# Kernel tuning notes

Measured on AMD Instinct MI355X. Metric: run time of the kernel, lower is better.

The kernel has to match this reference:

```python
import jax, jax.numpy as jnp
import numpy as np

ALPHA = 0.2  # leaky relu negative slope (LinearNet default)


def _init_linear(key, fan_in, fan_out):
    kw, kb = jax.random.split(key)
    lim = 1.0 / np.sqrt(fan_in)
    W = jax.random.uniform(kw, (fan_in, fan_out), jnp.float32, -lim, lim)
    b = jax.random.uniform(kb, (fan_out,), jnp.float32, -lim, lim)
    return W, b


def setup_inputs() -> dict:
    key = jax.random.key(0)
    keys = jax.random.split(key, 8)
    B, N, F = 8, 512, 32
    x = jax.random.normal(keys[0], (B, N, F), jnp.float32)
    # fe: [2F=64 -> 64 -> 64 -> 64], all layers leaky-relu (final_linear=False)
    fe_W0, fe_b0 = _init_linear(keys[1], 2 * F, 64)
    fe_W1, fe_b1 = _init_linear(keys[2], 64, 64)
    fe_W2, fe_b2 = _init_linear(keys[3], 64, 64)
    # fn: [64 + F = 96 -> 128 -> 128 -> 32], last layer linear (final_linear=True)
    fn_W0, fn_b0 = _init_linear(keys[4], 64 + F, 128)
    fn_W1, fn_b1 = _init_linear(keys[5], 128, 128)
    fn_W2, fn_b2 = _init_linear(keys[6], 128, 32)
    return {
        "x": x,
        "fe_W0": fe_W0, "fe_b0": fe_b0,
        "fe_W1": fe_W1, "fe_b1": fe_b1,
        "fe_W2": fe_W2, "fe_b2": fe_b2,
        "fn_W0": fn_W0, "fn_b0": fn_b0,
        "fn_W1": fn_W1, "fn_b1": fn_b1,
        "fn_W2": fn_W2, "fn_b2": fn_b2,
    }


def reference(x, fe_W0, fe_b0, fe_W1, fe_b1, fe_W2, fe_b2,
              fn_W0, fn_b0, fn_W1, fn_b1, fn_W2, fn_b2):
    B, N, F = x.shape
    # all-pairs edge inputs: A[b,i,j] = concat(x[b,i], x[b,j])  (x1=repeat rows, x2=tile)
    xi = jnp.broadcast_to(x[:, :, None, :], (B, N, N, F))
    xj = jnp.broadcast_to(x[:, None, :, :], (B, N, N, F))
    A = jnp.concatenate([xi, xj], axis=-1)  # [B, N, N, 2F]
    # edge MLP fe: leaky relu after every layer (final_linear=False)
    for W, b in ((fe_W0, fe_b0), (fe_W1, fe_b1), (fe_W2, fe_b2)):
        A = jax.nn.leaky_relu(A @ W + b, negative_slope=ALPHA)
    # sum aggregation over the sender axis j
    agg = jnp.sum(A, axis=2)  # [B, N, K]
    h = jnp.concatenate([agg, x], axis=-1)  # [B, N, K + F]
    # node MLP fn: leaky relu on hidden layers, final layer linear
    h = jax.nn.leaky_relu(h @ fn_W0 + fn_b0, negative_slope=ALPHA)
    h = jax.nn.leaky_relu(h @ fn_W1 + fn_b1, negative_slope=ALPHA)
    out = h @ fn_W2 + fn_b2  # [B, N, output_node_size]
    return out
```

## Files before the change

### kernel.cpp

```cpp
#include <hip/hip_runtime.h>
#include <hip/hip_bf16.h>

#define ALPHA 0.2f
static __device__ __forceinline__ float lrel(float x) { return fmaxf(x, ALPHA * x); }

typedef __attribute__((ext_vector_type(8))) short bf16x8;
typedef __attribute__((ext_vector_type(4))) float f32x4;

union FragU { bf16x8 v; unsigned int u[4]; uint4 q; };

static __device__ __forceinline__ unsigned int pk2(float a, float b) {
    unsigned int r;
    asm("v_cvt_pk_bf16_f32 %0, %1, %2" : "=v"(r) : "v"(a), "v"(b));
    return r;
}

__global__ __launch_bounds__(256) void k_uv(
    const float* __restrict__ x, const float* __restrict__ W0, const float* __restrict__ b0,
    const float* __restrict__ W1, const float* __restrict__ W2,
    float* __restrict__ U, float* __restrict__ V, unsigned int* __restrict__ WF)
{
    if (blockIdx.x == 1024) {
        const int t = threadIdx.x;
        const int l = t & 63, part = t >> 6;
        const int lo = l & 15, g = l >> 4;
#pragma unroll
        for (int q = 0; q < 2; ++q) {
            const int ff = part * 2 + q;
            const int s = ff >> 2, nf = ff & 3;
            const int pc = 32 * (nf >> 1) + 8 * (lo >> 2) + 4 * (nf & 1) + (lo & 3);
            const int c2 = 16 * nf + lo;
            unsigned int o1[4], o2[4];
#pragma unroll
            for (int uq = 0; uq < 4; ++uq) {
                const int k0 = 32 * s + 8 * g + 2 * uq;
                o1[uq] = pk2(W1[k0 * 64 + pc], W1[(k0 + 1) * 64 + pc]);
                o2[uq] = pk2(W2[k0 * 64 + c2], W2[(k0 + 1) * 64 + c2]);
            }
            *(uint4*)(WF + (ff * 64 + l) * 4)       = make_uint4(o1[0], o1[1], o1[2], o1[3]);
            *(uint4*)(WF + ((8 + ff) * 64 + l) * 4) = make_uint4(o2[0], o2[1], o2[2], o2[3]);
        }
        return;
    }
    int idx = blockIdx.x * 256 + threadIdx.x;
    int n = idx >> 6;
    int k = idx & 63;
    const float* xr = x + n * 32;
    float u = b0[k], v = 0.f;
#pragma unroll
    for (int f = 0; f < 32; ++f) {
        float xv = xr[f];
        u += xv * W0[f * 64 + k];
        v += xv * W0[(32 + f) * 64 + k];
    }
    U[idx] = u;
    V[idx] = v;
}

__global__ __launch_bounds__(256, 2) void k_edge(
    const float* __restrict__ U, const float* __restrict__ V,
    const unsigned int* __restrict__ WF,
    const float* __restrict__ b1, const float* __restrict__ b2,
    float* __restrict__ AGG)
{
    const int tid = threadIdx.x;
    const int w = tid >> 6, l = tid & 63;
    const int lo = l & 15, g = l >> 4;
    const int bid = blockIdx.x;
    const int b = bid >> 7, ig = bid & 127;
    const int i = ig * 4 + w;
    const int node = b * 512 + i;

    FragU w1f[2][4], w2f[2][4];
    const uint4* wp = (const uint4*)WF;
#pragma unroll
    for (int s = 0; s < 2; ++s)
#pragma unroll
        for (int nf = 0; nf < 4; ++nf) {
            w1f[s][nf].q = wp[(s * 4 + nf) * 64 + l];
            w2f[s][nf].q = wp[(8 + s * 4 + nf) * 64 + l];
        }

    f32x4 b1f[4], b2f[4];
#pragma unroll
    for (int nf = 0; nf < 4; ++nf) {
        const float4 t1 = *(const float4*)(b1 + 32 * (nf >> 1) + 8 * g + 4 * (nf & 1));
        const float4 t2 = *(const float4*)(b2 + 16 * nf + 4 * g);
        b1f[nf] = (f32x4){t1.x, t1.y, t1.z, t1.w};
        b2f[nf] = (f32x4){t2.x, t2.y, t2.z, t2.w};
    }

    const float* up = U + node * 64 + 8 * g;
    const float4 ua = *(const float4*)(up);
    const float4 ub = *(const float4*)(up + 4);
    const float4 uc = *(const float4*)(up + 32);
    const float4 ud = *(const float4*)(up + 36);

    const float* Vb = V + b * 512 * 64;
    float4 vaA, vbA, vcA, vdA, vaB, vbB, vcB, vdB;
    {
        const float* pA = Vb + lo * 64 + 8 * g;
        vaA = *(const float4*)(pA);      vbA = *(const float4*)(pA + 4);
        vcA = *(const float4*)(pA + 32); vdA = *(const float4*)(pA + 36);
        const float* pB = Vb + (16 + lo) * 64 + 8 * g;
        vaB = *(const float4*)(pB);      vbB = *(const float4*)(pB + 4);
        vcB = *(const float4*)(pB + 32); vdB = *(const float4*)(pB + 36);
    }

    f32x4 agg[4];
#pragma unroll
    for (int nf = 0; nf < 4; ++nf) { f32x4 z = {0.f, 0.f, 0.f, 0.f}; agg[nf] = z; }

#pragma unroll 1
    for (int jc = 0; jc < 512; jc += 32) {
        const int jn = (jc + 32 < 512) ? jc + 32 : 0;
        const float* pA = Vb + (jn + lo) * 64 + 8 * g;
        const float4 nvaA = *(const float4*)(pA);      const float4 nvbA = *(const float4*)(pA + 4);
        const float4 nvcA = *(const float4*)(pA + 32); const float4 nvdA = *(const float4*)(pA + 36);
        const float* pB = Vb + (jn + 16 + lo) * 64 + 8 * g;
        const float4 nvaB = *(const float4*)(pB);      const float4 nvbB = *(const float4*)(pB + 4);
        const float4 nvcB = *(const float4*)(pB + 32); const float4 nvdB = *(const float4*)(pB + 36);

        FragU h0aA, h0bA, h0aB, h0bB;
        h0aA.u[0] = pk2(lrel(ua.x + vaA.x), lrel(ua.y + vaA.y));
        h0aA.u[1] = pk2(lrel(ua.z + vaA.z), lrel(ua.w + vaA.w));
        h0aA.u[2] = pk2(lrel(ub.x + vbA.x), lrel(ub.y + vbA.y));
        h0aA.u[3] = pk2(lrel(ub.z + vbA.z), lrel(ub.w + vbA.w));
        h0bA.u[0] = pk2(lrel(uc.x + vcA.x), lrel(uc.y + vcA.y));
        h0bA.u[1] = pk2(lrel(uc.z + vcA.z), lrel(uc.w + vcA.w));
        h0bA.u[2] = pk2(lrel(ud.x + vdA.x), lrel(ud.y + vdA.y));
        h0bA.u[3] = pk2(lrel(ud.z + vdA.z), lrel(ud.w + vdA.w));
        h0aB.u[0] = pk2(lrel(ua.x + vaB.x), lrel(ua.y + vaB.y));
        h0aB.u[1] = pk2(lrel(ua.z + vaB.z), lrel(ua.w + vaB.w));
        h0aB.u[2] = pk2(lrel(ub.x + vbB.x), lrel(ub.y + vbB.y));
        h0aB.u[3] = pk2(lrel(ub.z + vbB.z), lrel(ub.w + vbB.w));
        h0bB.u[0] = pk2(lrel(uc.x + vcB.x), lrel(uc.y + vcB.y));
        h0bB.u[1] = pk2(lrel(uc.z + vcB.z), lrel(uc.w + vcB.w));
        h0bB.u[2] = pk2(lrel(ud.x + vdB.x), lrel(ud.y + vdB.y));
        h0bB.u[3] = pk2(lrel(ud.z + vdB.z), lrel(ud.w + vdB.w));

        f32x4 acc1A[4], acc1B[4];
#pragma unroll
        for (int nf = 0; nf < 4; ++nf) {
            acc1A[nf] = __builtin_amdgcn_mfma_f32_16x16x32_bf16(w1f[0][nf].v, h0aA.v, b1f[nf], 0, 0, 0);
            acc1B[nf] = __builtin_amdgcn_mfma_f32_16x16x32_bf16(w1f[0][nf].v, h0aB.v, b1f[nf], 0, 0, 0);
        }
#pragma unroll
        for (int nf = 0; nf < 4; ++nf) {
            acc1A[nf] = __builtin_amdgcn_mfma_f32_16x16x32_bf16(w1f[1][nf].v, h0bA.v, acc1A[nf], 0, 0, 0);
            acc1B[nf] = __builtin_amdgcn_mfma_f32_16x16x32_bf16(w1f[1][nf].v, h0bB.v, acc1B[nf], 0, 0, 0);
        }

        FragU p0A, p1A, p0B, p1B;
        p0A.u[0] = pk2(lrel(acc1A[0][0]), lrel(acc1A[0][1]));
        p0A.u[1] = pk2(lrel(acc1A[0][2]), lrel(acc1A[0][3]));
        p0A.u[2] = pk2(lrel(acc1A[1][0]), lrel(acc1A[1][1]));
        p0A.u[3] = pk2(lrel(acc1A[1][2]), lrel(acc1A[1][3]));
        p1A.u[0] = pk2(lrel(acc1A[2][0]), lrel(acc1A[2][1]));
        p1A.u[1] = pk2(lrel(acc1A[2][2]), lrel(acc1A[2][3]));
        p1A.u[2] = pk2(lrel(acc1A[3][0]), lrel(acc1A[3][1]));
        p1A.u[3] = pk2(lrel(acc1A[3][2]), lrel(acc1A[3][3]));
        p0B.u[0] = pk2(lrel(acc1B[0][0]), lrel(acc1B[0][1]));
        p0B.u[1] = pk2(lrel(acc1B[0][2]), lrel(acc1B[0][3]));
        p0B.u[2] = pk2(lrel(acc1B[1][0]), lrel(acc1B[1][1]));
        p0B.u[3] = pk2(lrel(acc1B[1][2]), lrel(acc1B[1][3]));
        p1B.u[0] = pk2(lrel(acc1B[2][0]), lrel(acc1B[2][1]));
        p1B.u[1] = pk2(lrel(acc1B[2][2]), lrel(acc1B[2][3]));
        p1B.u[2] = pk2(lrel(acc1B[3][0]), lrel(acc1B[3][1]));
        p1B.u[3] = pk2(lrel(acc1B[3][2]), lrel(acc1B[3][3]));

        f32x4 acc2A[4], acc2B[4];
#pragma unroll
        for (int nf = 0; nf < 4; ++nf) {
            acc2A[nf] = __builtin_amdgcn_mfma_f32_16x16x32_bf16(w2f[0][nf].v, p0A.v, b2f[nf], 0, 0, 0);
            acc2B[nf] = __builtin_amdgcn_mfma_f32_16x16x32_bf16(w2f[0][nf].v, p0B.v, b2f[nf], 0, 0, 0);
        }
#pragma unroll
        for (int nf = 0; nf < 4; ++nf) {
            acc2A[nf] = __builtin_amdgcn_mfma_f32_16x16x32_bf16(w2f[1][nf].v, p1A.v, acc2A[nf], 0, 0, 0);
            acc2B[nf] = __builtin_amdgcn_mfma_f32_16x16x32_bf16(w2f[1][nf].v, p1B.v, acc2B[nf], 0, 0, 0);
        }

#pragma unroll
        for (int nf = 0; nf < 4; ++nf)
#pragma unroll
            for (int r = 0; r < 4; ++r)
                agg[nf][r] += lrel(acc2A[nf][r]) + lrel(acc2B[nf][r]);

        vaA = nvaA; vbA = nvbA; vcA = nvcA; vdA = nvdA;
        vaB = nvaB; vbB = nvbB; vcB = nvcB; vdB = nvdB;
    }

#pragma unroll
    for (int nf = 0; nf < 4; ++nf)
#pragma unroll
        for (int r = 0; r < 4; ++r) {
            float v = agg[nf][r];
            v += __shfl_xor(v, 1);
            v += __shfl_xor(v, 2);
            v += __shfl_xor(v, 4);
            v += __shfl_xor(v, 8);
            agg[nf][r] = v;
        }
    if (lo == 0) {
#pragma unroll
        for (int nf = 0; nf < 4; ++nf) {
            float4 o = {agg[nf][0], agg[nf][1], agg[nf][2], agg[nf][3]};
            *(float4*)(AGG + node * 64 + 16 * nf + 4 * g) = o;
        }
    }
}

__global__ __launch_bounds__(256) void k_fn(
    const float* __restrict__ AGG, const float* __restrict__ x,
    const float* __restrict__ W0, const float* __restrict__ b0,
    const float* __restrict__ W1, const float* __restrict__ b1,
    const float* __restrict__ W2, const float* __restrict__ b2,
    float* __restrict__ out)
{
    __shared__ float in96T[96][8];
    __shared__ float h1T[128][8];
    __shared__ float h2T[128][8];
    const int t = threadIdx.x;
    const int half = t >> 7, f = t & 127;
    const int node0 = blockIdx.x * 8;

    for (int idx = t; idx < 768; idx += 256) {
        int nn = idx & 7, k = idx >> 3;
        in96T[k][nn] = (k < 64) ? AGG[(node0 + nn) * 64 + k]
                                : x[(node0 + nn) * 32 + (k - 64)];
    }
    __syncthreads();

    {
        float a0 = b0[f], a1 = a0, a2 = a0, a3 = a0;
#pragma unroll 4
        for (int k = 0; k < 96; ++k) {
            const float4 iv = *(const float4*)(&in96T[k][4 * half]);
            const float wv = W0[k * 128 + f];
            a0 += iv.x * wv; a1 += iv.y * wv; a2 += iv.z * wv; a3 += iv.w * wv;
        }
        float4 o = {lrel(a0), lrel(a1), lrel(a2), lrel(a3)};
        *(float4*)(&h1T[f][4 * half]) = o;
    }
    __syncthreads();

    {
        float a0 = b1[f], a1 = a0, a2 = a0, a3 = a0;
#pragma unroll 4
        for (int k = 0; k < 128; ++k) {
            const float4 iv = *(const float4*)(&h1T[k][4 * half]);
            const float wv = W1[k * 128 + f];
            a0 += iv.x * wv; a1 += iv.y * wv; a2 += iv.z * wv; a3 += iv.w * wv;
        }
        float4 o = {lrel(a0), lrel(a1), lrel(a2), lrel(a3)};
        *(float4*)(&h2T[f][4 * half]) = o;
    }
    __syncthreads();

    {
        const int nn = t >> 5, fo = t & 31;
        float a = b2[fo];
#pragma unroll 4
        for (int k = 0; k < 128; ++k) a += h2T[k][nn] * W2[k * 32 + fo];
        out[(node0 + nn) * 32 + fo] = a;
    }
}

extern "C" void kernel_launch(void* const* d_in, const int* in_sizes, int n_in,
                              void* d_out, int out_size, void* d_ws, size_t ws_size,
                              hipStream_t stream)
{
    const float* x    = (const float*)d_in[0];
    const float* feW0 = (const float*)d_in[1];
    const float* feb0 = (const float*)d_in[2];
    const float* feW1 = (const float*)d_in[3];
    const float* feb1 = (const float*)d_in[4];
    const float* feW2 = (const float*)d_in[5];
    const float* feb2 = (const float*)d_in[6];
    const float* fnW0 = (const float*)d_in[7];
    const float* fnb0 = (const float*)d_in[8];
    const float* fnW1 = (const float*)d_in[9];
    const float* fnb1 = (const float*)d_in[10];
    const float* fnW2 = (const float*)d_in[11];
    const float* fnb2 = (const float*)d_in[12];
    float* out = (float*)d_out;

    float* U   = (float*)d_ws;
    float* V   = U + 262144;
    float* AGG = V + 262144;
    unsigned int* WF = (unsigned int*)(AGG + 262144);

    hipLaunchKernelGGL(k_uv,   dim3(1025), dim3(256), 0, stream, x, feW0, feb0, feW1, feW2, U, V, WF);
    hipLaunchKernelGGL(k_edge, dim3(1024), dim3(256), 0, stream, U, V, WF, feb1, feb2, AGG);
    hipLaunchKernelGGL(k_fn,   dim3(512),  dim3(256), 0, stream, AGG, x, fnW0, fnb0, fnW1, fnb1, fnW2, fnb2, out);
}
```

Baseline: 85.67 us.

## Stage V tiles through swizzled LDS with double buffering and raise edge occupancy

The edge kernel now loads each 16-row V tile once per block into a double-buffered, XOR-swizzled shared-memory tile. Previously each wave read V rows straight from global memory, so the four waves of a block no longer fetch the same data separately. The loop processes 16 senders per iteration instead of 32, biases move from registers to LDS, and the elementwise leaky-relu and accumulate steps use packed f32 add/mul. Launch bounds are raised to 4 blocks per CU to cut register pressure and increase occupancy. The cost is a block-wide barrier every iteration, twice as many iterations, and extra LDS reads.

```diff
diff --git a/kernel.cpp b/kernel.cpp
--- a/kernel.cpp
+++ b/kernel.cpp
@@ -6,6 +6,7 @@
 
 typedef __attribute__((ext_vector_type(8))) short bf16x8;
 typedef __attribute__((ext_vector_type(4))) float f32x4;
+typedef __attribute__((ext_vector_type(2))) float f32x2;
 
 union FragU { bf16x8 v; unsigned int u[4]; uint4 q; };
 
@@ -13,6 +14,27 @@
     unsigned int r;
     asm("v_cvt_pk_bf16_f32 %0, %1, %2" : "=v"(r) : "v"(a), "v"(b));
     return r;
+}
+static __device__ __forceinline__ f32x2 mk2(float a, float b) { f32x2 r; r.x = a; r.y = b; return r; }
+static __device__ __forceinline__ f32x2 pkadd(f32x2 a, f32x2 b) {
+    f32x2 r;
+    asm("v_pk_add_f32 %0, %1, %2" : "=v"(r) : "v"(a), "v"(b));
+    return r;
+}
+static __device__ __forceinline__ f32x2 pkmul(f32x2 a, f32x2 b) {
+    f32x2 r;
+    asm("v_pk_mul_f32 %0, %1, %2" : "=v"(r) : "v"(a), "v"(b));
+    return r;
+}
+static __device__ __forceinline__ f32x2 lrel2(f32x2 x) {
+    f32x2 c; c.x = ALPHA; c.y = ALPHA;
+    f32x2 y = pkmul(x, c);
+    f32x2 r; r.x = fmaxf(x.x, y.x); r.y = fmaxf(x.y, y.y);
+    return r;
+}
+static __device__ __forceinline__ unsigned int cvl(f32x2 s) {
+    f32x2 l = lrel2(s);
+    return pk2(l.x, l.y);
 }
 
 __global__ __launch_bounds__(256) void k_uv(
@@ -57,19 +79,19 @@
     V[idx] = v;
 }
 
-__global__ __launch_bounds__(256, 2) void k_edge(
+__global__ __launch_bounds__(256, 4) void k_edge(
     const float* __restrict__ U, const float* __restrict__ V,
     const unsigned int* __restrict__ WF,
     const float* __restrict__ b1, const float* __restrict__ b2,
     float* __restrict__ AGG)
 {
+    __shared__ float lds[2176];
     const int tid = threadIdx.x;
     const int w = tid >> 6, l = tid & 63;
     const int lo = l & 15, g = l >> 4;
     const int bid = blockIdx.x;
     const int b = bid >> 7, ig = bid & 127;
-    const int i = ig * 4 + w;
-    const int node = b * 512 + i;
+    const int node = b * 512 + ig * 4 + w;
 
     FragU w1f[2][4], w2f[2][4];
     const uint4* wp = (const uint4*)WF;
@@ -81,13 +103,11 @@
             w2f[s][nf].q = wp[(8 + s * 4 + nf) * 64 + l];
         }
 
-    f32x4 b1f[4], b2f[4];
-#pragma unroll
-    for (int nf = 0; nf < 4; ++nf) {
-        const float4 t1 = *(const float4*)(b1 + 32 * (nf >> 1) + 8 * g + 4 * (nf & 1));
-        const float4 t2 = *(const float4*)(b2 + 16 * nf + 4 * g);
-        b1f[nf] = (f32x4){t1.x, t1.y, t1.z, t1.w};
-        b2f[nf] = (f32x4){t2.x, t2.y, t2.z, t2.w};
+    if (tid < 64) {
+        const int nf = tid >> 4, r4 = tid & 15;
+        const int gg = r4 >> 2, rr = r4 & 3;
+        lds[2048 + tid] = b1[32 * (nf >> 1) + 8 * gg + 4 * (nf & 1) + rr];
+        lds[2112 + tid] = b2[16 * nf + r4];
     }
 
     const float* up = U + node * 64 + 8 * g;
@@ -95,117 +115,109 @@
     const float4 ub = *(const float4*)(up + 4);
     const float4 uc = *(const float4*)(up + 32);
     const float4 ud = *(const float4*)(up + 36);
+    f32x2 u2[8];
+    u2[0] = mk2(ua.x, ua.y); u2[1] = mk2(ua.z, ua.w);
+    u2[2] = mk2(ub.x, ub.y); u2[3] = mk2(ub.z, ub.w);
+    u2[4] = mk2(uc.x, uc.y); u2[5] = mk2(uc.z, uc.w);
+    u2[6] = mk2(ud.x, ud.y); u2[7] = mk2(ud.z, ud.w);
 
     const float* Vb = V + b * 512 * 64;
-    float4 vaA, vbA, vcA, vdA, vaB, vbB, vcB, vdB;
+    const int wr = tid >> 4, wm = tid & 15;
+    const int woff = wr * 64 + ((wm ^ (wr & 7)) << 2);
+
     {
-        const float* pA = Vb + lo * 64 + 8 * g;
-        vaA = *(const float4*)(pA);      vbA = *(const float4*)(pA + 4);
-        vcA = *(const float4*)(pA + 32); vdA = *(const float4*)(pA + 36);
-        const float* pB = Vb + (16 + lo) * 64 + 8 * g;
-        vaB = *(const float4*)(pB);      vbB = *(const float4*)(pB + 4);
-        vcB = *(const float4*)(pB + 32); vdB = *(const float4*)(pB + 36);
-    }
-
-    f32x4 agg[4];
-#pragma unroll
-    for (int nf = 0; nf < 4; ++nf) { f32x4 z = {0.f, 0.f, 0.f, 0.f}; agg[nf] = z; }
+        const float4 nv = *(const float4*)(Vb + wr * 64 + wm * 4);
+        *(float4*)(lds + woff) = nv;
+    }
+    __syncthreads();
+
+    const int roff0 = lo * 64 + (((2 * g + 0) ^ (lo & 7)) << 2);
+    const int roff1 = lo * 64 + (((2 * g + 1) ^ (lo & 7)) << 2);
+    const int roff2 = lo * 64 + (((2 * g + 8) ^ (lo & 7)) << 2);
+    const int roff3 = lo * 64 + (((2 * g + 9) ^ (lo & 7)) << 2);
+
+    f32x2 agg2[4][2];
+#pragma unroll
+    for (int nf = 0; nf < 4; ++nf) { agg2[nf][0] = mk2(0.f, 0.f); agg2[nf][1] = mk2(0.f, 0.f); }
 
 #pragma unroll 1
-    for (int jc = 0; jc < 512; jc += 32) {
-        const int jn = (jc + 32 < 512) ? jc + 32 : 0;
-        const float* pA = Vb + (jn + lo) * 64 + 8 * g;
-        const float4 nvaA = *(const float4*)(pA);      const float4 nvbA = *(const float4*)(pA + 4);
-        const float4 nvcA = *(const float4*)(pA + 32); const float4 nvdA = *(const float4*)(pA + 36);
-        const float* pB = Vb + (jn + 16 + lo) * 64 + 8 * g;
-        const float4 nvaB = *(const float4*)(pB);      const float4 nvbB = *(const float4*)(pB + 4);
-        const float4 nvcB = *(const float4*)(pB + 32); const float4 nvdB = *(const float4*)(pB + 36);
-
-        FragU h0aA, h0bA, h0aB, h0bB;
-        h0aA.u[0] = pk2(lrel(ua.x + vaA.x), lrel(ua.y + vaA.y));
-        h0aA.u[1] = pk2(lrel(ua.z + vaA.z), lrel(ua.w + vaA.w));
-        h0aA.u[2] = pk2(lrel(ub.x + vbA.x), lrel(ub.y + vbA.y));
-        h0aA.u[3] = pk2(lrel(ub.z + vbA.z), lrel(ub.w + vbA.w));
-        h0bA.u[0] = pk2(lrel(uc.x + vcA.x), lrel(uc.y + vcA.y));
-        h0bA.u[1] = pk2(lrel(uc.z + vcA.z), lrel(uc.w + vcA.w));
-        h0bA.u[2] = pk2(lrel(ud.x + vdA.x), lrel(ud.y + vdA.y));
-        h0bA.u[3] = pk2(lrel(ud.z + vdA.z), lrel(ud.w + vdA.w));
-        h0aB.u[0] = pk2(lrel(ua.x + vaB.x), lrel(ua.y + vaB.y));
-        h0aB.u[1] = pk2(lrel(ua.z + vaB.z), lrel(ua.w + vaB.w));
-        h0aB.u[2] = pk2(lrel(ub.x + vbB.x), lrel(ub.y + vbB.y));
-        h0aB.u[3] = pk2(lrel(ub.z + vbB.z), lrel(ub.w + vbB.w));
-        h0bB.u[0] = pk2(lrel(uc.x + vcB.x), lrel(uc.y + vcB.y));
-        h0bB.u[1] = pk2(lrel(uc.z + vcB.z), lrel(uc.w + vcB.w));
-        h0bB.u[2] = pk2(lrel(ud.x + vdB.x), lrel(ud.y + vdB.y));
-        h0bB.u[3] = pk2(lrel(ud.z + vdB.z), lrel(ud.w + vdB.w));
-
-        f32x4 acc1A[4], acc1B[4];
-#pragma unroll
-        for (int nf = 0; nf < 4; ++nf) {
-            acc1A[nf] = __builtin_amdgcn_mfma_f32_16x16x32_bf16(w1f[0][nf].v, h0aA.v, b1f[nf], 0, 0, 0);
-            acc1B[nf] = __builtin_amdgcn_mfma_f32_16x16x32_bf16(w1f[0][nf].v, h0aB.v, b1f[nf], 0, 0, 0);
-        }
-#pragma unroll
-        for (int nf = 0; nf < 4; ++nf) {
-            acc1A[nf] = __builtin_amdgcn_mfma_f32_16x16x32_bf16(w1f[1][nf].v, h0bA.v, acc1A[nf], 0, 0, 0);
-            acc1B[nf] = __builtin_amdgcn_mfma_f32_16x16x32_bf16(w1f[1][nf].v, h0bB.v, acc1B[nf], 0, 0, 0);
-        }
-
-        FragU p0A, p1A, p0B, p1B;
-        p0A.u[0] = pk2(lrel(acc1A[0][0]), lrel(acc1A[0][1]));
-        p0A.u[1] = pk2(lrel(acc1A[0][2]), lrel(acc1A[0][3]));
-        p0A.u[2] = pk2(lrel(acc1A[1][0]), lrel(acc1A[1][1]));
-        p0A.u[3] = pk2(lrel(acc1A[1][2]), lrel(acc1A[1][3]));
-        p1A.u[0] = pk2(lrel(acc1A[2][0]), lrel(acc1A[2][1]));
-        p1A.u[1] = pk2(lrel(acc1A[2][2]), lrel(acc1A[2][3]));
-        p1A.u[2] = pk2(lrel(acc1A[3][0]), lrel(acc1A[3][1]));
-        p1A.u[3] = pk2(lrel(acc1A[3][2]), lrel(acc1A[3][3]));
-        p0B.u[0] = pk2(lrel(acc1B[0][0]), lrel(acc1B[0][1]));
-        p0B.u[1] = pk2(lrel(acc1B[0][2]), lrel(acc1B[0][3]));
-        p0B.u[2] = pk2(lrel(acc1B[1][0]), lrel(acc1B[1][1]));
-        p0B.u[3] = pk2(lrel(acc1B[1][2]), lrel(acc1B[1][3]));
-        p1B.u[0] = pk2(lrel(acc1B[2][0]), lrel(acc1B[2][1]));
-        p1B.u[1] = pk2(lrel(acc1B[2][2]), lrel(acc1B[2][3]));
-        p1B.u[2] = pk2(lrel(acc1B[3][0]), lrel(acc1B[3][1]));
-        p1B.u[3] = pk2(lrel(acc1B[3][2]), lrel(acc1B[3][3]));
-
-        f32x4 acc2A[4], acc2B[4];
-#pragma unroll
-        for (int nf = 0; nf < 4; ++nf) {
-            acc2A[nf] = __builtin_amdgcn_mfma_f32_16x16x32_bf16(w2f[0][nf].v, p0A.v, b2f[nf], 0, 0, 0);
-            acc2B[nf] = __builtin_amdgcn_mfma_f32_16x16x32_bf16(w2f[0][nf].v, p0B.v, b2f[nf], 0, 0, 0);
-        }
-#pragma unroll
-        for (int nf = 0; nf < 4; ++nf) {
-            acc2A[nf] = __builtin_amdgcn_mfma_f32_16x16x32_bf16(w2f[1][nf].v, p1A.v, acc2A[nf], 0, 0, 0);
-            acc2B[nf] = __builtin_amdgcn_mfma_f32_16x16x32_bf16(w2f[1][nf].v, p1B.v, acc2B[nf], 0, 0, 0);
-        }
-
-#pragma unroll
-        for (int nf = 0; nf < 4; ++nf)
-#pragma unroll
-            for (int r = 0; r < 4; ++r)
-                agg[nf][r] += lrel(acc2A[nf][r]) + lrel(acc2B[nf][r]);
-
-        vaA = nvaA; vbA = nvbA; vcA = nvcA; vdA = nvdA;
-        vaB = nvaB; vbB = nvbB; vcB = nvcB; vdB = nvdB;
-    }
-
+    for (int k = 0; k < 32; ++k) {
+        const int cur = (k & 1) << 10, nxt = ((k + 1) & 1) << 10;
+        const int jn = (k < 31) ? (k + 1) * 16 : 0;
+        const float4 nv = *(const float4*)(Vb + (jn + wr) * 64 + wm * 4);
+
+        const float4 va = *(const float4*)(lds + cur + roff0);
+        const float4 vb = *(const float4*)(lds + cur + roff1);
+        const float4 vc = *(const float4*)(lds + cur + roff2);
+        const float4 vd = *(const float4*)(lds + cur + roff3);
+
+        FragU A0, A1;
+        A0.u[0] = cvl(pkadd(u2[0], mk2(va.x, va.y)));
+        A0.u[1] = cvl(pkadd(u2[1], mk2(va.z, va.w)));
+        A0.u[2] = cvl(pkadd(u2[2], mk2(vb.x, vb.y)));
+        A0.u[3] = cvl(pkadd(u2[3], mk2(vb.z, vb.w)));
+        A1.u[0] = cvl(pkadd(u2[4], mk2(vc.x, vc.y)));
+        A1.u[1] = cvl(pkadd(u2[5], mk2(vc.z, vc.w)));
+        A1.u[2] = cvl(pkadd(u2[6], mk2(vd.x, vd.y)));
+        A1.u[3] = cvl(pkadd(u2[7], mk2(vd.z, vd.w)));
+
+        f32x4 acc1[4];
+#pragma unroll
+        for (int nf = 0; nf < 4; ++nf) {
+            const f32x4 c1 = *(const f32x4*)(lds + 2048 + nf * 16 + 4 * g);
+            acc1[nf] = __builtin_amdgcn_mfma_f32_16x16x32_bf16(w1f[0][nf].v, A0.v, c1, 0, 0, 0);
+            acc1[nf] = __builtin_amdgcn_mfma_f32_16x16x32_bf16(w1f[1][nf].v, A1.v, acc1[nf], 0, 0, 0);
+        }
+
+        FragU p0, p1;
+        p0.u[0] = cvl(mk2(acc1[0][0], acc1[0][1]));
+        p0.u[1] = cvl(mk2(acc1[0][2], acc1[0][3]));
+        p0.u[2] = cvl(mk2(acc1[1][0], acc1[1][1]));
+        p0.u[3] = cvl(mk2(acc1[1][2], acc1[1][3]));
+        p1.u[0] = cvl(mk2(acc1[2][0], acc1[2][1]));
+        p1.u[1] = cvl(mk2(acc1[2][2], acc1[2][3]));
+        p1.u[2] = cvl(mk2(acc1[3][0], acc1[3][1]));
+        p1.u[3] = cvl(mk2(acc1[3][2], acc1[3][3]));
+
+        f32x4 acc2[4];
+#pragma unroll
+        for (int nf = 0; nf < 4; ++nf) {
+            const f32x4 c2 = *(const f32x4*)(lds + 2112 + nf * 16 + 4 * g);
+            acc2[nf] = __builtin_amdgcn_mfma_f32_16x16x32_bf16(w2f[0][nf].v, p0.v, c2, 0, 0, 0);
+            acc2[nf] = __builtin_amdgcn_mfma_f32_16x16x32_bf16(w2f[1][nf].v, p1.v, acc2[nf], 0, 0, 0);
+        }
+
+#pragma unroll
+        for (int nf = 0; nf < 4; ++nf) {
+            agg2[nf][0] = pkadd(agg2[nf][0], lrel2(mk2(acc2[nf][0], acc2[nf][1])));
+            agg2[nf][1] = pkadd(agg2[nf][1], lrel2(mk2(acc2[nf][2], acc2[nf][3])));
+        }
+
+        *(float4*)(lds + nxt + woff) = nv;
+        __syncthreads();
+    }
+
+    float aggv[4][4];
+#pragma unroll
+    for (int nf = 0; nf < 4; ++nf) {
+        aggv[nf][0] = agg2[nf][0].x; aggv[nf][1] = agg2[nf][0].y;
+        aggv[nf][2] = agg2[nf][1].x; aggv[nf][3] = agg2[nf][1].y;
+    }
 #pragma unroll
     for (int nf = 0; nf < 4; ++nf)
 #pragma unroll
         for (int r = 0; r < 4; ++r) {
-            float v = agg[nf][r];
+            float v = aggv[nf][r];
             v += __shfl_xor(v, 1);
             v += __shfl_xor(v, 2);
             v += __shfl_xor(v, 4);
             v += __shfl_xor(v, 8);
-            agg[nf][r] = v;
+            aggv[nf][r] = v;
         }
     if (lo == 0) {
 #pragma unroll
         for (int nf = 0; nf < 4; ++nf) {
-            float4 o = {agg[nf][0], agg[nf][1], agg[nf][2], agg[nf][3]};
+            float4 o = {aggv[nf][0], aggv[nf][1], aggv[nf][2], aggv[nf][3]};
             *(float4*)(AGG + node * 64 + 16 * nf + 4 * g) = o;
         }
     }
```

Measured after the change: 111.3 us. 1.3x slower.
